# Performance work log

Measured on AMD Instinct MI355X. Metric: run time of the kernel, lower is better.

The kernel has to match this reference:

```python
import jax, jax.numpy as jnp
import numpy as np
from jax import lax

WAVELET_SCALES = 3


def _gaussian_filter(kernel_size):
    # matches torch init: x = arange(k) - k//2; w = exp(-x^2 / (2*(k/4)^2)); w /= w.sum()
    x = np.arange(kernel_size, dtype=np.float32) - kernel_size // 2
    w = np.exp(-x ** 2 / (2.0 * (kernel_size / 4.0) ** 2))
    return jnp.asarray(w / w.sum(), dtype=jnp.float32)


def setup_inputs() -> dict:
    key = jax.random.key(0)
    x = jax.random.normal(key, (32, 64, 8192), dtype=jnp.float32)
    return {
        "x": x,
        "w0": _gaussian_filter(3),
        "w1": _gaussian_filter(5),
        "w2": _gaussian_filter(7),
    }


def _conv1d_same(sig, w):
    # sig: [N, L], w: [k]; zero-padded cross-correlation (== torch Conv1d, no bias)
    k = w.shape[0]
    out = lax.conv_general_dilated(
        sig[:, None, :], w[None, None, :].astype(sig.dtype),
        window_strides=(1,), padding=[(k // 2, k // 2)],
        dimension_numbers=("NCH", "OIH", "NCH"))
    return out[:, 0, :]


def _avgpool2(sig):
    # kernel=2, stride=2 (L assumed even here, true for power-of-2 L)
    return 0.5 * (sig[..., ::2] + sig[..., 1::2])


def _interp_linear(sig, out_len):
    # F.interpolate(mode='linear', align_corners=False) on last axis
    in_len = sig.shape[-1]
    if in_len == out_len:
        return sig
    scale = in_len / out_len
    pos = (jnp.arange(out_len, dtype=jnp.float32) + 0.5) * scale - 0.5
    pos = jnp.clip(pos, 0.0, in_len - 1)
    lo = jnp.floor(pos).astype(jnp.int32)
    hi = jnp.minimum(lo + 1, in_len - 1)
    w = (pos - lo).astype(sig.dtype)
    return sig[..., lo] * (1.0 - w) + sig[..., hi] * w


def reference(x, w0, w1, w2):
    B, C, L0 = x.shape  # L0 >> 4, so the trivial small-L branch never triggers
    filters = [w0, w1, w2]
    sig = x.reshape(B * C, L0)
    L = L0
    coeffs = []
    for scale in range(WAVELET_SCALES):
        filtered = _conv1d_same(sig, filters[scale])  # [B*C, L]
        if scale > 0:
            # blur -> downsample by 2 -> linear-upsample back to current L
            coeff = _interp_linear(_avgpool2(filtered), L)
        else:
            coeff = filtered
        # resize every scale's coeff to the original length L0
        coeffs.append(_interp_linear(coeff, L0))
        if scale < WAVELET_SCALES - 1:
            sig = _avgpool2(sig)
            L = L // 2
    out = jnp.stack(coeffs, axis=1)  # [B*C, S, L0]
    return out.reshape(B, C, WAVELET_SCALES, L0)
```

## Files before the change

kernel.cpp:

```cpp
#include <hip/hip_runtime.h>

#define WT_L0 8192
#define WT_NT 512

typedef float f4 __attribute__((ext_vector_type(4)));
typedef float f2 __attribute__((ext_vector_type(2)));


__global__ __launch_bounds__(WT_NT) void wavelet1d_kernel(
    const float* __restrict__ x,
    const float* __restrict__ w0,
    const float* __restrict__ w1,
    const float* __restrict__ w2,
    float* __restrict__ out)
{
    __shared__ float buf[10240];
    const int row = blockIdx.x;
    const int t = threadIdx.x;
    const float* __restrict__ xr = x + (size_t)row * WT_L0;
    float* __restrict__ outr = out + (size_t)row * 3 * WT_L0;

    float f0[3], f1[5], f2a[7];
    #pragma unroll
    for (int k = 0; k < 3; ++k) f0[k] = w0[k];
    #pragma unroll
    for (int k = 0; k < 5; ++k) f1[k] = w1[k];
    #pragma unroll
    for (int k = 0; k < 7; ++k) f2a[k] = w2[k];

    {
        const f4* __restrict__ xr4 = (const f4*)xr;
        f4* __restrict__ out0_4 = (f4*)outr;
        f2* sig1_2 = (f2*)buf;
        #pragma unroll
        for (int c = 0; c < 4; ++c) {
            int q = t + 512 * c;
            f4 v = __builtin_nontemporal_load(&xr4[q]);
            float lm = (q > 0)    ? xr[4 * q - 1] : 0.f;
            float rp = (q < 2047) ? xr[4 * q + 4] : 0.f;
            f4 o;
            o.x = f0[0]*lm  + f0[1]*v.x + f0[2]*v.y;
            o.y = f0[0]*v.x + f0[1]*v.y + f0[2]*v.z;
            o.z = f0[0]*v.y + f0[1]*v.z + f0[2]*v.w;
            o.w = f0[0]*v.z + f0[1]*v.w + f0[2]*rp;
            __builtin_nontemporal_store(o, &out0_4[q]);
            f2 s; s.x = 0.5f * (v.x + v.y); s.y = 0.5f * (v.z + v.w);
            sig1_2[q] = s;
        }
    }
    __syncthreads();

    const float* sig1   = buf;
    const f4*    sig1_4 = (const f4*)sig1;

    {
        f4* filt1_4w = (f4*)(buf + 4096);
        f2* sig2_2   = (f2*)(buf + 8192);
        #pragma unroll
        for (int c = 0; c < 2; ++c) {
            int i = t + 512 * c;
            f4 v = sig1_4[i];
            f2 lf = (i > 0)    ? *(const f2*)&sig1[4 * i - 2] : (f2)(0.f);
            f2 rf = (i < 1023) ? *(const f2*)&sig1[4 * i + 4] : (f2)(0.f);
            f4 o;
            o.x = f1[0]*lf.x + f1[1]*lf.y + f1[2]*v.x  + f1[3]*v.y  + f1[4]*v.z;
            o.y = f1[0]*lf.y + f1[1]*v.x  + f1[2]*v.y  + f1[3]*v.z  + f1[4]*v.w;
            o.z = f1[0]*v.x  + f1[1]*v.y  + f1[2]*v.z  + f1[3]*v.w  + f1[4]*rf.x;
            o.w = f1[0]*v.y  + f1[1]*v.z  + f1[2]*v.w  + f1[3]*rf.x + f1[4]*rf.y;
            filt1_4w[i] = o;
            f2 s; s.x = 0.5f * (v.x + v.y); s.y = 0.5f * (v.z + v.w);
            sig2_2[i] = s;
        }
    }
    __syncthreads();

    const float* filt1   = buf + 4096;
    const f4*    filt1_4 = (const f4*)filt1;

    {
        f4* coeff1_4w = (f4*)buf;
        #pragma unroll
        for (int c = 0; c < 2; ++c) {
            int i = t + 512 * c;
            f4 v = filt1_4[i];
            float d1 = 0.5f * (v.x + v.y);
            float d2 = 0.5f * (v.z + v.w);
            float dm, dp;
            if (i > 0)    { f2 lf = *(const f2*)&filt1[4 * i - 2]; dm = 0.5f * (lf.x + lf.y); }
            else          { dm = d1; }
            if (i < 1023) { f2 rf = *(const f2*)&filt1[4 * i + 4]; dp = 0.5f * (rf.x + rf.y); }
            else          { dp = d2; }
            f4 o;
            o.x = 0.25f * dm + 0.75f * d1;
            o.y = 0.75f * d1 + 0.25f * d2;
            o.z = 0.25f * d1 + 0.75f * d2;
            o.w = 0.75f * d2 + 0.25f * dp;
            coeff1_4w[i] = o;
        }
    }
    __syncthreads();

    const float* coeff1 = buf;
    const float* sig2   = buf + 8192;
    const f4*    sig2_4 = (const f4*)sig2;

    {
        f4* __restrict__ out1_4 = (f4*)(outr + WT_L0);
        #pragma unroll
        for (int c = 0; c < 4; ++c) {
            int q = t + 512 * c;
            f2 c01 = *(const f2*)&coeff1[2 * q];
            float cm = (q > 0)    ? coeff1[2 * q - 1] : coeff1[0];
            float cp = (q < 2047) ? coeff1[2 * q + 2] : coeff1[4095];
            f4 o;
            o.x = 0.25f * cm    + 0.75f * c01.x;
            o.y = 0.75f * c01.x + 0.25f * c01.y;
            o.z = 0.25f * c01.x + 0.75f * c01.y;
            o.w = 0.75f * c01.y + 0.25f * cp;
            __builtin_nontemporal_store(o, &out1_4[q]);
        }
        f4* filt2_4w = (f4*)(buf + 4096);
        {
            int i = t;
            f4 v = sig2_4[i];
            float l3 = 0.f, l2 = 0.f, l1 = 0.f, r0 = 0.f, r1 = 0.f, r2 = 0.f;
            if (i > 0) {
                f2 lf = *(const f2*)&sig2[4 * i - 2];
                l3 = sig2[4 * i - 3]; l2 = lf.x; l1 = lf.y;
            }
            if (i < 511) {
                f2 rf = *(const f2*)&sig2[4 * i + 4];
                r0 = rf.x; r1 = rf.y; r2 = sig2[4 * i + 6];
            }
            f4 o;
            o.x = f2a[0]*l3  + f2a[1]*l2  + f2a[2]*l1  + f2a[3]*v.x + f2a[4]*v.y + f2a[5]*v.z + f2a[6]*v.w;
            o.y = f2a[0]*l2  + f2a[1]*l1  + f2a[2]*v.x + f2a[3]*v.y + f2a[4]*v.z + f2a[5]*v.w + f2a[6]*r0;
            o.z = f2a[0]*l1  + f2a[1]*v.x + f2a[2]*v.y + f2a[3]*v.z + f2a[4]*v.w + f2a[5]*r0  + f2a[6]*r1;
            o.w = f2a[0]*v.x + f2a[1]*v.y + f2a[2]*v.z + f2a[3]*v.w + f2a[4]*r0  + f2a[5]*r1  + f2a[6]*r2;
            filt2_4w[i] = o;
        }
    }
    __syncthreads();

    const float* filt2   = buf + 4096;
    const f4*    filt2_4 = (const f4*)filt2;

    {
        f4* coeff2_4w = (f4*)(buf + 6144);
        int i = t;
        f4 v = filt2_4[i];
        float d1 = 0.5f * (v.x + v.y);
        float d2 = 0.5f * (v.z + v.w);
        float dm, dp;
        if (i > 0)   { f2 lf = *(const f2*)&filt2[4 * i - 2]; dm = 0.5f * (lf.x + lf.y); }
        else         { dm = d1; }
        if (i < 511) { f2 rf = *(const f2*)&filt2[4 * i + 4]; dp = 0.5f * (rf.x + rf.y); }
        else         { dp = d2; }
        f4 o;
        o.x = 0.25f * dm + 0.75f * d1;
        o.y = 0.75f * d1 + 0.25f * d2;
        o.z = 0.25f * d1 + 0.75f * d2;
        o.w = 0.75f * d2 + 0.25f * dp;
        coeff2_4w[i] = o;
    }
    __syncthreads();

    const float* coeff2 = buf + 6144;

    {
        f4* __restrict__ out2_4 = (f4*)(outr + 2 * WT_L0);
        #pragma unroll
        for (int c = 0; c < 4; ++c) {
            int q = t + 512 * c;
            float c0 = coeff2[q];
            float cm = (q > 0)    ? coeff2[q - 1] : c0;
            float cp = (q < 2047) ? coeff2[q + 1] : c0;
            f4 o;
            o.x = 0.375f * cm + 0.625f * c0;
            o.y = 0.125f * cm + 0.875f * c0;
            o.z = 0.875f * c0 + 0.125f * cp;
            o.w = 0.625f * c0 + 0.375f * cp;
            __builtin_nontemporal_store(o, &out2_4[q]);
        }
    }
}

extern "C" void kernel_launch(void* const* d_in, const int* in_sizes, int n_in,
                              void* d_out, int out_size, void* d_ws, size_t ws_size,
                              hipStream_t stream) {
    const float* x  = (const float*)d_in[0];
    const float* w0 = (const float*)d_in[1];
    const float* w1 = (const float*)d_in[2];
    const float* w2 = (const float*)d_in[3];
    float* out = (float*)d_out;

    const int rows = in_sizes[0] / WT_L0;
    wavelet1d_kernel<<<dim3(rows), dim3(WT_NT), 0, stream>>>(x, w0, w1, w2, out);
}
```

Baseline: 51.73 us.

## Fuse blur+avgpool into strided filters and compose interpolations algebraically

Merges each scale's conv filter with the following 2x average pool into a longer combined filter evaluated only at downsampled positions. The chained linear upsamplings are collapsed into precomputed composite interpolation weights applied straight to the downsampled values. This drops two intermediate shared-memory stages and their barriers, and shrinks LDS use. The cost is different floating-point rounding and more complex, scalar LDS indexing in the level-2 filter.

```diff
diff --git a/kernel.cpp b/kernel.cpp
--- a/kernel.cpp
+++ b/kernel.cpp
@@ -14,7 +14,7 @@
     const float* __restrict__ w2,
     float* __restrict__ out)
 {
-    __shared__ float buf[10240];
+    __shared__ float buf[8192];
     const int row = blockIdx.x;
     const int t = threadIdx.x;
     const float* __restrict__ xr = x + (size_t)row * WT_L0;
@@ -27,6 +27,12 @@
     for (int k = 0; k < 5; ++k) f1[k] = w1[k];
     #pragma unroll
     for (int k = 0; k < 7; ++k) f2a[k] = w2[k];
+
+    const float g0 = 0.5f*f1[0], g1 = 0.5f*(f1[0]+f1[1]), g2 = 0.5f*(f1[1]+f1[2]),
+                g3 = 0.5f*(f1[2]+f1[3]), g4 = 0.5f*(f1[3]+f1[4]), g5 = 0.5f*f1[4];
+    const float h0 = 0.5f*f2a[0], h1 = 0.5f*(f2a[0]+f2a[1]), h2 = 0.5f*(f2a[1]+f2a[2]),
+                h3 = 0.5f*(f2a[2]+f2a[3]), h4 = 0.5f*(f2a[3]+f2a[4]),
+                h5 = 0.5f*(f2a[4]+f2a[5]), h6 = 0.5f*(f2a[5]+f2a[6]), h7 = 0.5f*f2a[6];
 
     {
         const f4* __restrict__ xr4 = (const f4*)xr;
@@ -54,132 +60,79 @@
     const f4*    sig1_4 = (const f4*)sig1;
 
     {
-        f4* filt1_4w = (f4*)(buf + 4096);
-        f2* sig2_2   = (f2*)(buf + 8192);
+        f2* down1_2 = (f2*)(buf + 4096);
+        f2* sig2_2  = (f2*)(buf + 6144);
         #pragma unroll
         for (int c = 0; c < 2; ++c) {
-            int i = t + 512 * c;
-            f4 v = sig1_4[i];
-            f2 lf = (i > 0)    ? *(const f2*)&sig1[4 * i - 2] : (f2)(0.f);
-            f2 rf = (i < 1023) ? *(const f2*)&sig1[4 * i + 4] : (f2)(0.f);
-            f4 o;
-            o.x = f1[0]*lf.x + f1[1]*lf.y + f1[2]*v.x  + f1[3]*v.y  + f1[4]*v.z;
-            o.y = f1[0]*lf.y + f1[1]*v.x  + f1[2]*v.y  + f1[3]*v.z  + f1[4]*v.w;
-            o.z = f1[0]*v.x  + f1[1]*v.y  + f1[2]*v.z  + f1[3]*v.w  + f1[4]*rf.x;
-            o.w = f1[0]*v.y  + f1[1]*v.z  + f1[2]*v.w  + f1[3]*rf.x + f1[4]*rf.y;
-            filt1_4w[i] = o;
+            int j = t + 512 * c;
+            f4 v = sig1_4[j];
+            f2 lf = (j > 0)    ? *(const f2*)&sig1[4 * j - 2] : (f2)(0.f);
+            f2 rf = (j < 1023) ? *(const f2*)&sig1[4 * j + 4] : (f2)(0.f);
+            f2 d;
+            d.x = g0*lf.x + g1*lf.y + g2*v.x + g3*v.y + g4*v.z + g5*v.w;
+            d.y = g0*v.x  + g1*v.y  + g2*v.z + g3*v.w + g4*rf.x + g5*rf.y;
+            down1_2[j] = d;
             f2 s; s.x = 0.5f * (v.x + v.y); s.y = 0.5f * (v.z + v.w);
-            sig2_2[i] = s;
+            sig2_2[j] = s;
         }
     }
     __syncthreads();
 
-    const float* filt1   = buf + 4096;
-    const f4*    filt1_4 = (const f4*)filt1;
-
-    {
-        f4* coeff1_4w = (f4*)buf;
-        #pragma unroll
-        for (int c = 0; c < 2; ++c) {
-            int i = t + 512 * c;
-            f4 v = filt1_4[i];
-            float d1 = 0.5f * (v.x + v.y);
-            float d2 = 0.5f * (v.z + v.w);
-            float dm, dp;
-            if (i > 0)    { f2 lf = *(const f2*)&filt1[4 * i - 2]; dm = 0.5f * (lf.x + lf.y); }
-            else          { dm = d1; }
-            if (i < 1023) { f2 rf = *(const f2*)&filt1[4 * i + 4]; dp = 0.5f * (rf.x + rf.y); }
-            else          { dp = d2; }
-            f4 o;
-            o.x = 0.25f * dm + 0.75f * d1;
-            o.y = 0.75f * d1 + 0.25f * d2;
-            o.z = 0.25f * d1 + 0.75f * d2;
-            o.w = 0.75f * d2 + 0.25f * dp;
-            coeff1_4w[i] = o;
-        }
-    }
-    __syncthreads();
-
-    const float* coeff1 = buf;
-    const float* sig2   = buf + 8192;
-    const f4*    sig2_4 = (const f4*)sig2;
+    const float* down1 = buf + 4096;
+    const float* sig2  = buf + 6144;
 
     {
         f4* __restrict__ out1_4 = (f4*)(outr + WT_L0);
         #pragma unroll
         for (int c = 0; c < 4; ++c) {
             int q = t + 512 * c;
-            f2 c01 = *(const f2*)&coeff1[2 * q];
-            float cm = (q > 0)    ? coeff1[2 * q - 1] : coeff1[0];
-            float cp = (q < 2047) ? coeff1[2 * q + 2] : coeff1[4095];
+            float d0  = down1[q];
+            float dm1 = (q > 0)    ? down1[q - 1] : d0;
+            float d1  = (q < 2047) ? down1[q + 1] : d0;
             f4 o;
-            o.x = 0.25f * cm    + 0.75f * c01.x;
-            o.y = 0.75f * c01.x + 0.25f * c01.y;
-            o.z = 0.25f * c01.x + 0.75f * c01.y;
-            o.w = 0.75f * c01.y + 0.25f * cp;
+            o.x = 0.375f  * dm1 + 0.625f * d0;
+            o.y = 0.1875f * dm1 + 0.75f  * d0 + 0.0625f * d1;
+            o.z = 0.0625f * dm1 + 0.75f  * d0 + 0.1875f * d1;
+            o.w = 0.625f  * d0  + 0.375f * d1;
             __builtin_nontemporal_store(o, &out1_4[q]);
         }
-        f4* filt2_4w = (f4*)(buf + 4096);
-        {
-            int i = t;
-            f4 v = sig2_4[i];
-            float l3 = 0.f, l2 = 0.f, l1 = 0.f, r0 = 0.f, r1 = 0.f, r2 = 0.f;
-            if (i > 0) {
-                f2 lf = *(const f2*)&sig2[4 * i - 2];
-                l3 = sig2[4 * i - 3]; l2 = lf.x; l1 = lf.y;
-            }
-            if (i < 511) {
-                f2 rf = *(const f2*)&sig2[4 * i + 4];
-                r0 = rf.x; r1 = rf.y; r2 = sig2[4 * i + 6];
-            }
-            f4 o;
-            o.x = f2a[0]*l3  + f2a[1]*l2  + f2a[2]*l1  + f2a[3]*v.x + f2a[4]*v.y + f2a[5]*v.z + f2a[6]*v.w;
-            o.y = f2a[0]*l2  + f2a[1]*l1  + f2a[2]*v.x + f2a[3]*v.y + f2a[4]*v.z + f2a[5]*v.w + f2a[6]*r0;
-            o.z = f2a[0]*l1  + f2a[1]*v.x + f2a[2]*v.y + f2a[3]*v.z + f2a[4]*v.w + f2a[5]*r0  + f2a[6]*r1;
-            o.w = f2a[0]*v.x + f2a[1]*v.y + f2a[2]*v.z + f2a[3]*v.w + f2a[4]*r0  + f2a[5]*r1  + f2a[6]*r2;
-            filt2_4w[i] = o;
+        float* down2 = buf;
+        #pragma unroll
+        for (int c = 0; c < 2; ++c) {
+            int j = t + 512 * c;
+            int base = 2 * j - 3;
+            float s0 = (base + 0 >= 0)   ? sig2[base + 0] : 0.f;
+            float s1 = (base + 1 >= 0)   ? sig2[base + 1] : 0.f;
+            float s2 = (base + 2 >= 0)   ? sig2[base + 2] : 0.f;
+            float s3 = sig2[base + 3];
+            float s4 = sig2[base + 4];
+            float s5 = (base + 5 < 2048) ? sig2[base + 5] : 0.f;
+            float s6 = (base + 6 < 2048) ? sig2[base + 6] : 0.f;
+            float s7 = (base + 7 < 2048) ? sig2[base + 7] : 0.f;
+            down2[j] = h0*s0 + h1*s1 + h2*s2 + h3*s3 + h4*s4 + h5*s5 + h6*s6 + h7*s7;
         }
     }
     __syncthreads();
 
-    const float* filt2   = buf + 4096;
-    const f4*    filt2_4 = (const f4*)filt2;
-
-    {
-        f4* coeff2_4w = (f4*)(buf + 6144);
-        int i = t;
-        f4 v = filt2_4[i];
-        float d1 = 0.5f * (v.x + v.y);
-        float d2 = 0.5f * (v.z + v.w);
-        float dm, dp;
-        if (i > 0)   { f2 lf = *(const f2*)&filt2[4 * i - 2]; dm = 0.5f * (lf.x + lf.y); }
-        else         { dm = d1; }
-        if (i < 511) { f2 rf = *(const f2*)&filt2[4 * i + 4]; dp = 0.5f * (rf.x + rf.y); }
-        else         { dp = d2; }
-        f4 o;
-        o.x = 0.25f * dm + 0.75f * d1;
-        o.y = 0.75f * d1 + 0.25f * d2;
-        o.z = 0.25f * d1 + 0.75f * d2;
-        o.w = 0.75f * d2 + 0.25f * dp;
-        coeff2_4w[i] = o;
-    }
-    __syncthreads();
-
-    const float* coeff2 = buf + 6144;
+    const float* down2 = buf;
 
     {
         f4* __restrict__ out2_4 = (f4*)(outr + 2 * WT_L0);
         #pragma unroll
         for (int c = 0; c < 4; ++c) {
             int q = t + 512 * c;
-            float c0 = coeff2[q];
-            float cm = (q > 0)    ? coeff2[q - 1] : c0;
-            float cp = (q < 2047) ? coeff2[q + 1] : c0;
-            f4 o;
-            o.x = 0.375f * cm + 0.625f * c0;
-            o.y = 0.125f * cm + 0.875f * c0;
-            o.z = 0.875f * c0 + 0.125f * cp;
-            o.w = 0.625f * c0 + 0.375f * cp;
+            int m = q >> 1;
+            int p = q & 1;
+            float d0  = down2[m];
+            float dm1 = (m > 0)    ? down2[m - 1] : d0;
+            float d1  = (m < 1023) ? down2[m + 1] : d0;
+            f4 wa = p ? (f4){0.09375f, 0.03125f, 0.f,      0.f     }
+                      : (f4){0.4375f,  0.3125f,  0.21875f, 0.15625f};
+            f4 wb = p ? (f4){0.75f,    0.75f,    0.6875f,  0.5625f }
+                      : (f4){0.5625f,  0.6875f,  0.75f,    0.75f   };
+            f4 wc = p ? (f4){0.15625f, 0.21875f, 0.3125f,  0.4375f }
+                      : (f4){0.f,      0.f,      0.03125f, 0.09375f};
+            f4 o = wa * dm1 + wb * d0 + wc * d1;
             __builtin_nontemporal_store(o, &out2_4[q]);
         }
     }
```

New measurement: 52.92 us. 2.3% more time.
